# Kernel tuning notes

Hardware: AMD Instinct MI355X
Metric: run time of the kernel (lower is better)

Reference implementation:

```python
import jax, jax.numpy as jnp
import numpy as np
from jax import lax

HEAD_NUM = 16
QKV_DIM = 16
TOP_K = 2
SQRT_EMBED = 16.0   # sqrt_embedding_dim for E=256
LOGIT_CLIP = 10.0


def setup_inputs() -> dict:
    key = jax.random.key(0)
    ks = jax.random.split(key, 12)
    B, P, N1, E, HD, NE = 256, 100, 101, 256, 256, 8
    s = 0.05
    return {
        "encoded_last_node": jax.random.normal(ks[0], (B, P, E), jnp.float32),
        "attr": jax.random.uniform(ks[1], (B, P, 4), jnp.float32),
        "encoded_nodes": jax.random.normal(ks[2], (B, N1, E), jnp.float32),
        "ninf_mask": jnp.zeros((B, P, N1), jnp.float32),
        "attention_bias": jax.random.normal(ks[3], (B, P, N1), jnp.float32),
        "attention_bias1": jax.random.normal(ks[4], (B, P, N1), jnp.float32),
        "Wq_last": jax.random.normal(ks[5], (E + 4, HD), jnp.float32) * s,
        "Wk": jax.random.normal(ks[6], (E, HD), jnp.float32) * s,
        "Wv": jax.random.normal(ks[7], (E, HD), jnp.float32) * s,
        "Wg": jax.random.normal(ks[8], (HD, NE), jnp.float32) * s,
        "expert_W": jax.random.normal(ks[9], (NE, HD, E), jnp.float32) * s,
        "expert_b": jnp.zeros((NE, E), jnp.float32),
    }


def _heads(x, H, D):
    B, n, _ = x.shape
    return x.reshape(B, n, H, D).transpose(0, 2, 1, 3)  # (B,H,n,D)


def reference(encoded_last_node, attr, encoded_nodes, ninf_mask,
              attention_bias, attention_bias1, Wq_last, Wk, Wv,
              Wg, expert_W, expert_b):
    B, P, E = encoded_last_node.shape
    H, D = HEAD_NUM, QKV_DIM
    # q from [last_node ; attr], k/v from encoded_nodes (set_kv)
    q = _heads(jnp.concatenate([encoded_last_node, attr], axis=-1) @ Wq_last, H, D)
    k = _heads(encoded_nodes @ Wk, H, D)   # (B,H,N+1,D)
    v = _heads(encoded_nodes @ Wv, H, D)
    inv_sqrt_d = 1.0 / jnp.sqrt(jnp.asarray(D, jnp.float32))
    score = jnp.einsum('bhpd,bhnd->bhpn', q, k) * inv_sqrt_d
    score = score + ninf_mask[:, None, :, :]           # rank3 ninf mask
    w = jax.nn.softmax(score, axis=-1)
    out = jnp.einsum('bhpn,bhnd->bhpd', w, v)
    out_concat = out.transpose(0, 2, 1, 3).reshape(B, P, H * D)
    # --- top-k gated MoE combine (node-level routing, eval path) ---
    x = out_concat.reshape(B * P, H * D)               # tokens
    logits = x @ Wg                                    # (T, NE)
    top_v, top_i = lax.top_k(logits, TOP_K)
    top_g = jax.nn.softmax(top_v, axis=-1)
    gates = jnp.zeros_like(logits).at[
        jnp.arange(x.shape[0])[:, None], top_i].set(top_g)   # (T, NE)
    expert_out = jnp.einsum('tf,efo->teo', x, expert_W) + expert_b[None]
    mh = jnp.einsum('teo,te->to', expert_out, gates).reshape(B, P, E)
    # --- single-head pointer scores with bias + tanh clipping ---
    score2 = jnp.einsum('bpe,bne->bpn', mh, encoded_nodes)
    score2 = score2 + attention_bias + attention_bias1
    score2 = LOGIT_CLIP * jnp.tanh(score2 / SQRT_EMBED)
    probs = jax.nn.softmax(score2 + ninf_mask, axis=-1)  # (B,P,N+1)
    return probs
```

## Files before the change

### kernel.cpp

```cpp
#include <hip/hip_runtime.h>
#include <hip/hip_bf16.h>

#define B   256
#define P   100
#define N1  101
#define E   256
#define HD  256
#define H   16
#define D   16
#define NE  8
#define NTOK (B*P)
#define NKV  (B*N1)

typedef __attribute__((ext_vector_type(8))) short short8;
typedef __attribute__((ext_vector_type(4))) float f32x4;
typedef unsigned short ushort_t;

__device__ __forceinline__ unsigned short f2bf(float f) {
  unsigned int u = __float_as_uint(f);
  unsigned int r = (u + 0x7fffu + ((u >> 16) & 1u)) >> 16;
  return (unsigned short)r;
}
__device__ __forceinline__ float bf2f(unsigned short b) {
  return __uint_as_float(((unsigned int)b) << 16);
}
__device__ __forceinline__ unsigned int cvtpk(float a, float b) {
  unsigned int r;
  asm("v_cvt_pk_bf16_f32 %0, %1, %2" : "=v"(r) : "v"(a), "v"(b));
  return r;
}
__device__ __forceinline__ float lo2f(unsigned int u) {
  return __uint_as_float(u << 16);
}
__device__ __forceinline__ float hi2f(unsigned int u) {
  return __uint_as_float(u & 0xffff0000u);
}

__device__ __forceinline__ void split3_pack(const float* v, uint4& uh,
                                            uint4& um, uint4& ul) {
  unsigned int hw[4], mw[4], lw[4];
#pragma unroll
  for (int jj = 0; jj < 4; ++jj) {
    float va = v[2 * jj], vb = v[2 * jj + 1];
    unsigned int h = cvtpk(va, vb);
    float ra = va - lo2f(h), rb = vb - hi2f(h);
    unsigned int m = cvtpk(ra, rb);
    float sa = ra - lo2f(m), sb = rb - hi2f(m);
    unsigned int l = cvtpk(sa, sb);
    hw[jj] = h; mw[jj] = m; lw[jj] = l;
  }
  uh.x = hw[0]; uh.y = hw[1]; uh.z = hw[2]; uh.w = hw[3];
  um.x = mw[0]; um.y = mw[1]; um.z = mw[2]; um.w = mw[3];
  ul.x = lw[0]; ul.y = lw[1]; ul.z = lw[2]; ul.w = lw[3];
}

__global__ __launch_bounds__(256) void wsplit3_kernel(
    const float* __restrict__ W, uint4* __restrict__ Wp, int Kreal) {
  const int gid = blockIdx.x * 256 + threadIdx.x;
  const int lane = gid & 63;
  const int rest = gid >> 6;
  const int gct = rest & 15;
  const int kt = rest >> 4;
  const int k0 = kt * 32 + (lane >> 4) * 8;
  const int c = gct * 16 + (lane & 15);
  float v[8];
#pragma unroll
  for (int j = 0; j < 8; ++j) {
    int kk = k0 + j;
    v[j] = (kk < Kreal) ? W[(size_t)kk * 256 + c] : 0.f;
  }
  uint4 uh, um, ul;
  split3_pack(v, uh, um, ul);
  Wp[(size_t)(rest * 3 + 0) * 64 + lane] = uh;
  Wp[(size_t)(rest * 3 + 1) * 64 + lane] = um;
  Wp[(size_t)(rest * 3 + 2) * 64 + lane] = ul;
}

__global__ __launch_bounds__(256) void kvproj3_kernel(
    const float* __restrict__ enc, const uint4* __restrict__ Wk3,
    const uint4* __restrict__ Wv3, float* __restrict__ kout,
    float* __restrict__ vout) {
  const int KT = 8;
  const int NKG = KT * 4;
  const int RSTRIDE = KT * 12 + 1;
  __shared__ uint4 als[32 * 97];
  const int tid = threadIdx.x;
  const int row0 = blockIdx.x * 32;
  for (int i = tid; i < 32 * NKG; i += 256) {
    const int row = i >> 5;
    const int kg = i & 31;
    float v[8];
    const float4* s = (const float4*)(enc + (size_t)(row0 + row) * 256 + kg * 8);
    float4 x0 = s[0], x1 = s[1];
    v[0] = x0.x; v[1] = x0.y; v[2] = x0.z; v[3] = x0.w;
    v[4] = x1.x; v[5] = x1.y; v[6] = x1.z; v[7] = x1.w;
    uint4 uh, um, ul;
    split3_pack(v, uh, um, ul);
    const int slot = row * RSTRIDE + kg;
    als[slot] = uh;
    als[slot + NKG] = um;
    als[slot + 2 * NKG] = ul;
  }
  __syncthreads();
  const int w = tid >> 6;
  const int lane = tid & 63;
  const int lr = lane & 15;
  const int lg4 = lane >> 4;
  f32x4 acck[2][4], accv[2][4];
#pragma unroll
  for (int rt = 0; rt < 2; ++rt)
#pragma unroll
    for (int ct = 0; ct < 4; ++ct) {
      acck[rt][ct] = (f32x4){0.f, 0.f, 0.f, 0.f};
      accv[rt][ct] = (f32x4){0.f, 0.f, 0.f, 0.f};
    }
  for (int kt = 0; kt < KT; ++kt) {
    short8 ah[2], am[2], al[2];
#pragma unroll
    for (int rt = 0; rt < 2; ++rt) {
      const int base = (rt * 16 + lr) * RSTRIDE + kt * 4 + lg4;
      ah[rt] = __builtin_bit_cast(short8, als[base]);
      am[rt] = __builtin_bit_cast(short8, als[base + NKG]);
      al[rt] = __builtin_bit_cast(short8, als[base + 2 * NKG]);
    }
#pragma unroll
    for (int ct = 0; ct < 4; ++ct) {
      const int gct = w * 4 + ct;
      const size_t base = (size_t)((kt * 16 + gct) * 3) * 64 + lane;
      {
        short8 bh = __builtin_bit_cast(short8, Wk3[base]);
        short8 bm = __builtin_bit_cast(short8, Wk3[base + 64]);
        short8 bl = __builtin_bit_cast(short8, Wk3[base + 128]);
#pragma unroll
        for (int rt = 0; rt < 2; ++rt) {
          f32x4 a = acck[rt][ct];
          a = __builtin_amdgcn_mfma_f32_16x16x32_bf16(ah[rt], bh, a, 0, 0, 0);
          a = __builtin_amdgcn_mfma_f32_16x16x32_bf16(ah[rt], bm, a, 0, 0, 0);
          a = __builtin_amdgcn_mfma_f32_16x16x32_bf16(am[rt], bh, a, 0, 0, 0);
          a = __builtin_amdgcn_mfma_f32_16x16x32_bf16(am[rt], bm, a, 0, 0, 0);
          a = __builtin_amdgcn_mfma_f32_16x16x32_bf16(ah[rt], bl, a, 0, 0, 0);
          a = __builtin_amdgcn_mfma_f32_16x16x32_bf16(al[rt], bh, a, 0, 0, 0);
          acck[rt][ct] = a;
        }
      }
      {
        short8 bh = __builtin_bit_cast(short8, Wv3[base]);
        short8 bm = __builtin_bit_cast(short8, Wv3[base + 64]);
        short8 bl = __builtin_bit_cast(short8, Wv3[base + 128]);
#pragma unroll
        for (int rt = 0; rt < 2; ++rt) {
          f32x4 a = accv[rt][ct];
          a = __builtin_amdgcn_mfma_f32_16x16x32_bf16(ah[rt], bh, a, 0, 0, 0);
          a = __builtin_amdgcn_mfma_f32_16x16x32_bf16(ah[rt], bm, a, 0, 0, 0);
          a = __builtin_amdgcn_mfma_f32_16x16x32_bf16(am[rt], bh, a, 0, 0, 0);
          a = __builtin_amdgcn_mfma_f32_16x16x32_bf16(am[rt], bm, a, 0, 0, 0);
          a = __builtin_amdgcn_mfma_f32_16x16x32_bf16(ah[rt], bl, a, 0, 0, 0);
          a = __builtin_amdgcn_mfma_f32_16x16x32_bf16(al[rt], bh, a, 0, 0, 0);
          accv[rt][ct] = a;
        }
      }
    }
  }
#pragma unroll
  for (int rt = 0; rt < 2; ++rt) {
#pragma unroll
    for (int ct = 0; ct < 4; ++ct) {
      const int gct = w * 4 + ct;
#pragma unroll
      for (int reg = 0; reg < 4; ++reg) {
        const int row = row0 + rt * 16 + lg4 * 4 + reg;
        int bb = row / N1, nn = row - bb * N1;
        size_t o = (((size_t)bb * H + gct) * N1 + nn) * D + lr;
        kout[o] = acck[rt][ct][reg];
        vout[o] = accv[rt][ct][reg];
      }
    }
  }
}

template <int KT, int MODE>
__global__ __launch_bounds__(256) void proj3_kernel(
    const float* __restrict__ src, const float* __restrict__ attr,
    const uint4* __restrict__ Wp3, float* __restrict__ outp) {
  const int RSTRIDE = KT * 12 + 1;
  __shared__ uint4 als[32 * (KT * 12 + 1)];
  const int tid = threadIdx.x;
  const int row0 = blockIdx.x * 32;
  const int NKG = KT * 4;
  for (int i = tid; i < 32 * NKG; i += 256) {
    const int row = i / NKG;
    const int kg = i - row * NKG;
    float v[8];
    const int kbase = kg * 8;
    if (MODE == 0 || kbase < 256) {
      const float4* s = (const float4*)(src + (size_t)(row0 + row) * 256 + kbase);
      float4 x0 = s[0], x1 = s[1];
      v[0] = x0.x; v[1] = x0.y; v[2] = x0.z; v[3] = x0.w;
      v[4] = x1.x; v[5] = x1.y; v[6] = x1.z; v[7] = x1.w;
    } else {
#pragma unroll
      for (int j = 0; j < 8; ++j) {
        int k = kbase + j;
        v[j] = (k >= 256 && k < 260) ? attr[(size_t)(row0 + row) * 4 + (k - 256)]
                                     : 0.f;
      }
    }
    uint4 uh, um, ul;
    split3_pack(v, uh, um, ul);
    const int slot = row * RSTRIDE + kg;
    als[slot] = uh;
    als[slot + NKG] = um;
    als[slot + 2 * NKG] = ul;
  }
  __syncthreads();
  const int w = tid >> 6;
  const int lane = tid & 63;
  const int lr = lane & 15;
  const int lg4 = lane >> 4;
  f32x4 acc[2][4];
#pragma unroll
  for (int rt = 0; rt < 2; ++rt)
#pragma unroll
    for (int ct = 0; ct < 4; ++ct) acc[rt][ct] = (f32x4){0.f, 0.f, 0.f, 0.f};
  for (int kt = 0; kt < KT; ++kt) {
    short8 ah[2], am[2], al[2];
#pragma unroll
    for (int rt = 0; rt < 2; ++rt) {
      const int base = (rt * 16 + lr) * RSTRIDE + kt * 4 + lg4;
      ah[rt] = __builtin_bit_cast(short8, als[base]);
      am[rt] = __builtin_bit_cast(short8, als[base + NKG]);
      al[rt] = __builtin_bit_cast(short8, als[base + 2 * NKG]);
    }
#pragma unroll
    for (int ct = 0; ct < 4; ++ct) {
      const int gct = w * 4 + ct;
      const size_t base = (size_t)((kt * 16 + gct) * 3) * 64 + lane;
      short8 bh = __builtin_bit_cast(short8, Wp3[base]);
      short8 bm = __builtin_bit_cast(short8, Wp3[base + 64]);
      short8 bl = __builtin_bit_cast(short8, Wp3[base + 128]);
#pragma unroll
      for (int rt = 0; rt < 2; ++rt) {
        f32x4 a = acc[rt][ct];
        a = __builtin_amdgcn_mfma_f32_16x16x32_bf16(ah[rt], bh, a, 0, 0, 0);
        a = __builtin_amdgcn_mfma_f32_16x16x32_bf16(ah[rt], bm, a, 0, 0, 0);
        a = __builtin_amdgcn_mfma_f32_16x16x32_bf16(am[rt], bh, a, 0, 0, 0);
        a = __builtin_amdgcn_mfma_f32_16x16x32_bf16(am[rt], bm, a, 0, 0, 0);
        a = __builtin_amdgcn_mfma_f32_16x16x32_bf16(ah[rt], bl, a, 0, 0, 0);
        a = __builtin_amdgcn_mfma_f32_16x16x32_bf16(al[rt], bh, a, 0, 0, 0);
        acc[rt][ct] = a;
      }
    }
  }
#pragma unroll
  for (int rt = 0; rt < 2; ++rt) {
#pragma unroll
    for (int ct = 0; ct < 4; ++ct) {
      const int gct = w * 4 + ct;
#pragma unroll
      for (int reg = 0; reg < 4; ++reg) {
        const int row = row0 + rt * 16 + lg4 * 4 + reg;
        size_t o;
        if (MODE == 0) {
          int bb = row / N1, nn = row - bb * N1;
          o = (((size_t)bb * H + gct) * N1 + nn) * D + lr;
        } else {
          int bb = row / P, pp = row - bb * P;
          o = (((size_t)bb * H + gct) * P + pp) * D + lr;
        }
        outp[o] = acc[rt][ct][reg];
      }
    }
  }
}

__device__ __forceinline__ float dot16f(
    const float4& a0, const float4& a1, const float4& a2, const float4& a3,
    const float4& b0, const float4& b1, const float4& b2, const float4& b3) {
  float s = a0.x * b0.x;
  s = fmaf(a0.y, b0.y, s); s = fmaf(a0.z, b0.z, s); s = fmaf(a0.w, b0.w, s);
  s = fmaf(a1.x, b1.x, s); s = fmaf(a1.y, b1.y, s); s = fmaf(a1.z, b1.z, s);
  s = fmaf(a1.w, b1.w, s);
  s = fmaf(a2.x, b2.x, s); s = fmaf(a2.y, b2.y, s); s = fmaf(a2.z, b2.z, s);
  s = fmaf(a2.w, b2.w, s);
  s = fmaf(a3.x, b3.x, s); s = fmaf(a3.y, b3.y, s); s = fmaf(a3.z, b3.z, s);
  s = fmaf(a3.w, b3.w, s);
  return s;
}

__global__ __launch_bounds__(256) void attn_kernel(
    const float* __restrict__ q, const float* __restrict__ k,
    const float* __restrict__ v, const float* __restrict__ ninf,
    float* __restrict__ x) {
  const int b = blockIdx.x >> 3;
  const int h0 = (blockIdx.x & 7) * 2;
  __shared__ float4 kl4[2 * 208];
  __shared__ float4 vl4[2 * 208];
  const int tid = threadIdx.x;
  const int w = tid >> 6;
  const int lane = tid & 63;
  const int hh = w >> 1;
  const int h = h0 + hh;
  const int prow = (w & 1) * 64 + lane;
  const bool act = (prow < P);
  const int p = act ? prow : (P - 1);
  const float LOG2E = 1.4426950408889634f;
  const float c1 = 0.25f * LOG2E;
  const float* qb = q + (((size_t)b * H + h) * P + p) * D;
  float4 qa0 = *(const float4*)&qb[0];
  float4 qa1 = *(const float4*)&qb[4];
  float4 qa2 = *(const float4*)&qb[8];
  float4 qa3 = *(const float4*)&qb[12];
  qa0.x *= c1; qa0.y *= c1; qa0.z *= c1; qa0.w *= c1;
  qa1.x *= c1; qa1.y *= c1; qa1.z *= c1; qa1.w *= c1;
  qa2.x *= c1; qa2.y *= c1; qa2.z *= c1; qa2.w *= c1;
  qa3.x *= c1; qa3.y *= c1; qa3.z *= c1; qa3.w *= c1;
  const float* mrow = ninf + ((size_t)b * P + p) * N1;
  const float* kw = (const float*)(kl4 + hh * 208);
  const float* vw = (const float*)(vl4 + hh * 208);

  float m2 = -1e30f, l = 0.f;
  float o[16];
#pragma unroll
  for (int d = 0; d < 16; ++d) o[d] = 0.f;

#pragma unroll
  for (int ch = 0; ch < 2; ++ch) {
    const int c0 = ch ? 52 : 0;
    const int len = ch ? 49 : 52;
    const int nf4 = len * 4;
    __syncthreads();
    for (int i = tid; i < 2 * nf4; i += 256) {
      int hs = i / nf4, rem = i - hs * nf4;
      const float4* ks =
          (const float4*)(k + (((size_t)b * H + h0 + hs) * N1 + c0) * D);
      const float4* vs =
          (const float4*)(v + (((size_t)b * H + h0 + hs) * N1 + c0) * D);
      kl4[hs * 208 + rem] = ks[rem];
      vl4[hs * 208 + rem] = vs[rem];
    }
    __syncthreads();
    const int nit = len >> 2;
    float4 mk = *(const float4*)&mrow[c0];
    for (int it = 0; it < nit; ++it) {
      const int j = it * 4;
      const int nn = (it < nit - 1) ? (c0 + j + 4) : c0;
      float4 nx = *(const float4*)&mrow[nn];
      const float4* kr0 = (const float4*)&kw[(j + 0) * D];
      const float4* kr1 = (const float4*)&kw[(j + 1) * D];
      const float4* kr2 = (const float4*)&kw[(j + 2) * D];
      const float4* kr3 = (const float4*)&kw[(j + 3) * D];
      float4 k00 = kr0[0], k01 = kr0[1], k02 = kr0[2], k03 = kr0[3];
      float4 k10 = kr1[0], k11 = kr1[1], k12 = kr1[2], k13 = kr1[3];
      float4 k20 = kr2[0], k21 = kr2[1], k22 = kr2[2], k23 = kr2[3];
      float4 k30 = kr3[0], k31 = kr3[1], k32 = kr3[2], k33 = kr3[3];
      float s0 = fmaf(mk.x, LOG2E, dot16f(qa0, qa1, qa2, qa3, k00, k01, k02, k03));
      float s1 = fmaf(mk.y, LOG2E, dot16f(qa0, qa1, qa2, qa3, k10, k11, k12, k13));
      float s2 = fmaf(mk.z, LOG2E, dot16f(qa0, qa1, qa2, qa3, k20, k21, k22, k23));
      float s3 = fmaf(mk.w, LOG2E, dot16f(qa0, qa1, qa2, qa3, k30, k31, k32, k33));
      float mn = fmaxf(fmaxf(fmaxf(s0, s1), fmaxf(s2, s3)), m2);
      float sc = exp2f(m2 - mn);
      float p0 = exp2f(s0 - mn), p1 = exp2f(s1 - mn);
      float p2 = exp2f(s2 - mn), p3 = exp2f(s3 - mn);
      l = fmaf(l, sc, (p0 + p1) + (p2 + p3));
      const float4* vr0 = (const float4*)&vw[(j + 0) * D];
      const float4* vr1 = (const float4*)&vw[(j + 1) * D];
      const float4* vr2 = (const float4*)&vw[(j + 2) * D];
      const float4* vr3 = (const float4*)&vw[(j + 3) * D];
#pragma unroll
      for (int dq = 0; dq < 4; ++dq) {
        float4 v0 = vr0[dq], v1 = vr1[dq], v2 = vr2[dq], v3 = vr3[dq];
        o[4 * dq + 0] = fmaf(o[4 * dq + 0], sc,
            fmaf(p0, v0.x, fmaf(p1, v1.x, fmaf(p2, v2.x, p3 * v3.x))));
        o[4 * dq + 1] = fmaf(o[4 * dq + 1], sc,
            fmaf(p0, v0.y, fmaf(p1, v1.y, fmaf(p2, v2.y, p3 * v3.y))));
        o[4 * dq + 2] = fmaf(o[4 * dq + 2], sc,
            fmaf(p0, v0.z, fmaf(p1, v1.z, fmaf(p2, v2.z, p3 * v3.z))));
        o[4 * dq + 3] = fmaf(o[4 * dq + 3], sc,
            fmaf(p0, v0.w, fmaf(p1, v1.w, fmaf(p2, v2.w, p3 * v3.w))));
      }
      m2 = mn;
      mk = nx;
    }
  }
  {
    const float tm = mrow[100];
    const float4* kr = (const float4*)&kw[48 * D];
    float4 k0 = kr[0], k1 = kr[1], k2 = kr[2], k3 = kr[3];
    float s = fmaf(tm, LOG2E, dot16f(qa0, qa1, qa2, qa3, k0, k1, k2, k3));
    float mn = fmaxf(m2, s);
    float sc = exp2f(m2 - mn);
    float pp = exp2f(s - mn);
    l = fmaf(l, sc, pp);
    const float4* vr = (const float4*)&vw[48 * D];
#pragma unroll
    for (int dq = 0; dq < 4; ++dq) {
      float4 v0 = vr[dq];
      o[4 * dq + 0] = fmaf(o[4 * dq + 0], sc, pp * v0.x);
      o[4 * dq + 1] = fmaf(o[4 * dq + 1], sc, pp * v0.y);
      o[4 * dq + 2] = fmaf(o[4 * dq + 2], sc, pp * v0.z);
      o[4 * dq + 3] = fmaf(o[4 * dq + 3], sc, pp * v0.w);
    }
  }
  if (act) {
    const float inv = 1.f / l;
    float* xr = &x[((size_t)b * P + p) * HD + h * D];
#pragma unroll
    for (int dq = 0; dq < 4; ++dq) {
      float4 t;
      t.x = o[4 * dq + 0] * inv; t.y = o[4 * dq + 1] * inv;
      t.z = o[4 * dq + 2] * inv; t.w = o[4 * dq + 3] * inv;
      *(float4*)&xr[4 * dq] = t;
    }
  }
}

__global__ __launch_bounds__(256) void logits_top2_kernel(
    const float* __restrict__ x, const float* __restrict__ Wg,
    int* __restrict__ topi, float* __restrict__ topg,
    ushort_t* __restrict__ xsplit) {
  __shared__ float xl[32][260];
  __shared__ float wg[E * NE];
  __shared__ float lg[32][9];
  const int tid = threadIdx.x;
  const int t0 = blockIdx.x * 32;
  for (int r = 0; r < 32; ++r) {
    float val = x[(size_t)(t0 + r) * HD + tid];
    xl[r][tid] = val;
    unsigned short hi = f2bf(val);
    unsigned short lo = f2bf(val - bf2f(hi));
    xsplit[(size_t)(t0 + r) * 512 + tid] = hi;
    xsplit[(size_t)(t0 + r) * 512 + 256 + tid] = lo;
  }
  for (int i = tid; i < E * NE; i += 256) wg[i] = Wg[i];
  __syncthreads();
  const int r = tid >> 3, e = tid & 7;
  float acc = 0.f;
  for (int f = 0; f < E; ++f) acc += xl[r][f] * wg[f * NE + e];
  lg[r][e] = acc;
  __syncthreads();
  if (tid < 32) {
    float v[8];
#pragma unroll
    for (int j = 0; j < 8; ++j) v[j] = lg[tid][j];
    int i1 = 0; float v1 = v[0];
#pragma unroll
    for (int j = 1; j < 8; ++j) if (v[j] > v1) { v1 = v[j]; i1 = j; }
    int i2 = -1; float v2 = -1e30f;
#pragma unroll
    for (int j = 0; j < 8; ++j)
      if (j != i1 && v[j] > v2) { v2 = v[j]; i2 = j; }
    float ex = __expf(v2 - v1);
    float g1 = 1.f / (1.f + ex);
    float g2 = ex / (1.f + ex);
    int t = t0 + tid;
    topi[t * 2 + 0] = i1; topi[t * 2 + 1] = i2;
    topg[t * 2 + 0] = g1; topg[t * 2 + 1] = g2;
  }
}

__global__ __launch_bounds__(1024) void build_lists_kernel(
    const int* __restrict__ topi, const float* __restrict__ topg,
    int* __restrict__ list_tok, float* __restrict__ list_gate,
    int* __restrict__ counts) {
  const int e = blockIdx.x;
  const int tid = threadIdx.x;
  const int lane = tid & 63, w = tid >> 6;
  __shared__ int wsum[16];
  int running = 0;
  for (int c = 0; c < NTOK; c += 1024) {
    int t = c + tid;
    int ia = topi[t * 2 + 0], ib = topi[t * 2 + 1];
    int slot = (ia == e) ? 0 : ((ib == e) ? 1 : -1);
    int f = (slot >= 0) ? 1 : 0;
    unsigned long long m = __ballot(f);
    if (lane == 0) wsum[w] = __popcll(m);
    __syncthreads();
    int wbase = 0, total = 0;
#pragma unroll
    for (int i = 0; i < 16; ++i) {
      int s = wsum[i];
      if (i < w) wbase += s;
      total += s;
    }
    if (f) {
      int prefix = __popcll(m & ((1ull << lane) - 1ull));
      int pos = running + wbase + prefix;
      list_tok[e * NTOK + pos] = (t << 1) | slot;
      list_gate[e * NTOK + pos] = topg[t * 2 + slot];
    }
    running += total;
    __syncthreads();
  }
  if (tid == 0) counts[e] = running;
}

__global__ __launch_bounds__(256) void wsplit_kernel(
    const float* __restrict__ eW, uint4* __restrict__ Wp) {
  const int gid = blockIdx.x * 256 + threadIdx.x;
  const int lane = gid & 63;
  const int rest = gid >> 6;
  const int gct = rest & 15;
  const int kt = (rest >> 4) & 7;
  const int e = rest >> 7;
  const int kbase = kt * 32 + (lane >> 4) * 8;
  const int c = gct * 16 + (lane & 15);
  unsigned int hi[4], lo[4];
#pragma unroll
  for (int jj = 0; jj < 4; ++jj) {
    float v0 = eW[((size_t)e * HD + (kbase + 2 * jj)) * E + c];
    float v1 = eW[((size_t)e * HD + (kbase + 2 * jj + 1)) * E + c];
    unsigned int h = cvtpk(v0, v1);
    float r0 = v0 - lo2f(h), r1 = v1 - hi2f(h);
    unsigned int l = cvtpk(r0, r1);
    hi[jj] = h; lo[jj] = l;
  }
  uint4 uh, ul;
  uh.x = hi[0]; uh.y = hi[1]; uh.z = hi[2]; uh.w = hi[3];
  ul.x = lo[0]; ul.y = lo[1]; ul.z = lo[2]; ul.w = lo[3];
  Wp[(size_t)(rest * 2 + 0) * 64 + lane] = uh;
  Wp[(size_t)(rest * 2 + 1) * 64 + lane] = ul;
}

__global__ __launch_bounds__(256) void expert_gemm_kernel(
    const ushort_t* __restrict__ xsplit, const uint4* __restrict__ Wp,
    const float* __restrict__ eb, const int* __restrict__ list_tok,
    const float* __restrict__ list_gate, const int* __restrict__ counts,
    float* __restrict__ p0, float* __restrict__ p1) {
  int e = 0, t0 = -1;
  {
    int rem = blockIdx.x;
    for (int i = 0; i < NE; ++i) {
      int nt = (counts[i] + 47) / 48;
      if (rem < nt) { e = i; t0 = rem * 48; break; }
      rem -= nt;
    }
  }
  if (t0 < 0) return;
  const int cnt = counts[e];
  const int nr = min(48, cnt - t0);
  __shared__ uint4 xls[48 * 65];
  __shared__ int stok[48];
  __shared__ float sg[48];
  const int tid = threadIdx.x;
  if (tid < 48) {
    int src = e * NTOK + t0 + ((tid < nr) ? tid : 0);
    stok[tid] = list_tok[src];
    sg[tid] = (tid < nr) ? list_gate[e * NTOK + t0 + tid] : 0.f;
  }
  __syncthreads();
  for (int i = tid; i < 48 * 64; i += 256) {
    int r = i >> 6, ch = i & 63;
    const uint4* src = (const uint4*)(xsplit + (size_t)(stok[r] >> 1) * 512);
    xls[r * 65 + ch] = src[ch];
  }
  __syncthreads();
  const int w = tid >> 6;
  const int lane = tid & 63;
  const int lr = lane & 15;
  const int lg4 = lane >> 4;
  f32x4 acc[3][4];
#pragma unroll
  for (int rt = 0; rt < 3; ++rt)
#pragma unroll
    for (int ct = 0; ct < 4; ++ct) acc[rt][ct] = (f32x4){0.f, 0.f, 0.f, 0.f};

  for (int kt = 0; kt < 8; ++kt) {
    short8 afrag[3][2];
#pragma unroll
    for (int rt = 0; rt < 3; ++rt)
#pragma unroll
      for (int pl = 0; pl < 2; ++pl) {
        uint4 u = xls[(rt * 16 + lr) * 65 + pl * 32 + kt * 4 + lg4];
        afrag[rt][pl] = __builtin_bit_cast(short8, u);
      }
#pragma unroll
    for (int ct = 0; ct < 4; ++ct) {
      const int gct = w * 4 + ct;
      const size_t base = (size_t)(((e * 8 + kt) * 16 + gct) * 2) * 64 + lane;
      short8 bh = __builtin_bit_cast(short8, Wp[base]);
      short8 bl = __builtin_bit_cast(short8, Wp[base + 64]);
#pragma unroll
      for (int rt = 0; rt < 3; ++rt) {
        acc[rt][ct] = __builtin_amdgcn_mfma_f32_16x16x32_bf16(
            afrag[rt][0], bh, acc[rt][ct], 0, 0, 0);
        acc[rt][ct] = __builtin_amdgcn_mfma_f32_16x16x32_bf16(
            afrag[rt][0], bl, acc[rt][ct], 0, 0, 0);
        acc[rt][ct] = __builtin_amdgcn_mfma_f32_16x16x32_bf16(
            afrag[rt][1], bh, acc[rt][ct], 0, 0, 0);
      }
    }
  }
#pragma unroll
  for (int rt = 0; rt < 3; ++rt) {
#pragma unroll
    for (int ct = 0; ct < 4; ++ct) {
      const int col = (w * 4 + ct) * 16 + lr;
      const float bias = eb[e * E + col];
#pragma unroll
      for (int reg = 0; reg < 4; ++reg) {
        const int ridx = rt * 16 + lg4 * 4 + reg;
        if (ridx < nr) {
          const int tokw = stok[ridx];
          const float g = sg[ridx];
          float* dst = ((tokw & 1) ? p1 : p0) + (size_t)(tokw >> 1) * E + col;
          *dst = g * (acc[rt][ct][reg] + bias);
        }
      }
    }
  }
}

__global__ __launch_bounds__(256) void score2_fused_kernel(
    const float* __restrict__ p0, const float* __restrict__ p1,
    const float* __restrict__ enc, const float* __restrict__ ab,
    const float* __restrict__ ab1, const float* __restrict__ ninf,
    float* __restrict__ out) {
  const int b = blockIdx.x >> 1;
  const int half = blockIdx.x & 1;
  const int r0 = half * 50;
  __shared__ float4 mh4[50 * 64];
  const int tid = threadIdx.x;
  for (int i = tid; i < 50 * 64; i += 256) {
    int r = i >> 6, c4 = i & 63;
    size_t idx = (size_t)(b * P + r0 + r) * 64 + c4;
    float4 a = ((const float4*)p0)[idx];
    float4 c = ((const float4*)p1)[idx];
    float4 s;
    s.x = a.x + c.x; s.y = a.y + c.y; s.z = a.z + c.z; s.w = a.w + c.w;
    mh4[i] = s;
  }
  __syncthreads();
  const int w = tid >> 6;
  const int lane = tid & 63;
  const int n0 = lane;
  const int n1v = lane + 64;
  const bool has1 = (n1v < N1);
  const int n1 = has1 ? n1v : (N1 - 1);
  const float4* er0 = (const float4*)(enc + ((size_t)b * N1 + n0) * E);
  const float4* er1 = (const float4*)(enc + ((size_t)b * N1 + n1) * E);
  float acc0[13], acc1[13];
#pragma unroll
  for (int j = 0; j < 13; ++j) { acc0[j] = 0.f; acc1[j] = 0.f; }
  for (int kk = 0; kk < 64; ++kk) {
    float4 e0 = er0[kk];
    float4 e1 = er1[kk];
#pragma unroll
    for (int j = 0; j < 13; ++j) {
      const int r = w + j * 4;
      if (r < 50) {
        float4 mv = mh4[r * 64 + kk];
        acc0[j] = fmaf(mv.w, e0.w,
                  fmaf(mv.z, e0.z, fmaf(mv.y, e0.y, fmaf(mv.x, e0.x, acc0[j]))));
        acc1[j] = fmaf(mv.w, e1.w,
                  fmaf(mv.z, e1.z, fmaf(mv.y, e1.y, fmaf(mv.x, e1.x, acc1[j]))));
      }
    }
  }
#pragma unroll
  for (int j = 0; j < 13; ++j) {
    const int r = w + j * 4;
    if (r < 50) {
      const int prow = b * P + r0 + r;
      const float* arow = ab + (size_t)prow * N1;
      const float* a1row = ab1 + (size_t)prow * N1;
      const float* nrow = ninf + (size_t)prow * N1;
      float s0 = acc0[j] + arow[n0] + a1row[n0];
      float e20 = __expf(s0 * 0.125f);
      float v0 = 10.f - 20.f / (e20 + 1.f) + nrow[n0];
      float v1 = -1e30f;
      if (has1) {
        float s1 = acc1[j] + arow[n1v] + a1row[n1v];
        float e21 = __expf(s1 * 0.125f);
        v1 = 10.f - 20.f / (e21 + 1.f) + nrow[n1v];
      }
      float mx = fmaxf(v0, v1);
#pragma unroll
      for (int off = 32; off > 0; off >>= 1)
        mx = fmaxf(mx, __shfl_xor(mx, off, 64));
      float q0 = __expf(v0 - mx);
      float q1 = has1 ? __expf(v1 - mx) : 0.f;
      float sum = q0 + q1;
#pragma unroll
      for (int off = 32; off > 0; off >>= 1)
        sum += __shfl_xor(sum, off, 64);
      float inv = 1.f / sum;
      float* orow = out + (size_t)prow * N1;
      orow[n0] = q0 * inv;
      if (has1) orow[n1v] = q1 * inv;
    }
  }
}

extern "C" void kernel_launch(void* const* d_in, const int* in_sizes, int n_in,
                              void* d_out, int out_size, void* d_ws,
                              size_t ws_size, hipStream_t stream) {
  const float* eln  = (const float*)d_in[0];
  const float* attr = (const float*)d_in[1];
  const float* enc  = (const float*)d_in[2];
  const float* ninf = (const float*)d_in[3];
  const float* ab   = (const float*)d_in[4];
  const float* ab1  = (const float*)d_in[5];
  const float* Wq   = (const float*)d_in[6];
  const float* Wk   = (const float*)d_in[7];
  const float* Wv   = (const float*)d_in[8];
  const float* Wg   = (const float*)d_in[9];
  const float* eW   = (const float*)d_in[10];
  const float* eb   = (const float*)d_in[11];
  float* out = (float*)d_out;

  char* ws = (char*)d_ws;
  size_t off = 0;
  auto carve = [&](size_t bytes) {
    char* p = ws + off;
    off += (bytes + 255) & ~size_t(255);
    return p;
  };
  float* kbuf = (float*)carve(sizeof(float) * NKV * HD);
  float* vbuf = (float*)carve(sizeof(float) * NKV * HD);
  float* qbuf = (float*)carve(sizeof(float) * NTOK * HD);
  float* xbuf = (float*)carve(sizeof(float) * NTOK * HD);
  int*   topi = (int*)carve(sizeof(int) * NTOK * 2);
  float* topg = (float*)carve(sizeof(float) * NTOK * 2);
  int*   counts = (int*)carve(sizeof(int) * 16);
  int*   list_tok = (int*)carve(sizeof(int) * NE * NTOK);
  float* list_gate = (float*)carve(sizeof(float) * NE * NTOK);
  uint4* Wp  = (uint4*)carve(sizeof(ushort_t) * NE * HD * E * 2);
  uint4* Wk3 = (uint4*)carve((size_t)8 * 16 * 3 * 64 * 16);
  uint4* Wv3 = (uint4*)carve((size_t)8 * 16 * 3 * 64 * 16);
  uint4* Wq3 = (uint4*)carve((size_t)9 * 16 * 3 * 64 * 16);
  float* pp0 = kbuf;
  float* pp1 = vbuf;
  ushort_t* xsplit = (ushort_t*)qbuf;

  wsplit_kernel<<<256, 256, 0, stream>>>(eW, Wp);
  wsplit3_kernel<<<32, 256, 0, stream>>>(Wk, Wk3, 256);
  wsplit3_kernel<<<32, 256, 0, stream>>>(Wv, Wv3, 256);
  wsplit3_kernel<<<36, 256, 0, stream>>>(Wq, Wq3, 260);
  kvproj3_kernel<<<NKV / 32, 256, 0, stream>>>(enc, Wk3, Wv3, kbuf, vbuf);
  proj3_kernel<9, 1><<<NTOK / 32, 256, 0, stream>>>(eln, attr, Wq3, qbuf);
  attn_kernel<<<B * 8, 256, 0, stream>>>(qbuf, kbuf, vbuf, ninf, xbuf);
  logits_top2_kernel<<<NTOK / 32, 256, 0, stream>>>(xbuf, Wg, topi, topg,
                                                    xsplit);
  build_lists_kernel<<<NE, 1024, 0, stream>>>(topi, topg, list_tok, list_gate,
                                              counts);
  expert_gemm_kernel<<<1075, 256, 0, stream>>>(xsplit, Wp, eb, list_tok,
                                               list_gate, counts, pp0, pp1);
  score2_fused_kernel<<<512, 256, 0, stream>>>(pp0, pp1, enc, ab, ab1, ninf,
                                               out);
}
```

Measured before the change: 319.0 us.

## Merge weight-split kernels, add lazy softmax rescale, parallelize MoE list building

Four weight-preprocessing launches become one prep kernel dispatched by block index, which saves launch overhead. The attention inner loop skips the online-softmax rescale unless some lane's new max beats the running max by more than a threshold, cutting exp and multiply work. The gating logits kernel transposes Wg in shared memory for vectorized float4 dot products. The single-pass 8-block list builder is replaced by a count/scan/scatter sequence over 200 chunks, which adds parallelism but also two extra launches, and the ordering within expert lists changes.

Result: faster. 298.2 us (-6.5%).

```diff
diff --git a/kernel.cpp b/kernel.cpp
--- a/kernel.cpp
+++ b/kernel.cpp
@@ -11,6 +11,8 @@
 #define NE  8
 #define NTOK (B*P)
 #define NKV  (B*N1)
+#define NCHK 200
+#define CHKSZ 128
 
 typedef __attribute__((ext_vector_type(8))) short short8;
 typedef __attribute__((ext_vector_type(4))) float f32x4;
@@ -54,9 +56,9 @@
   ul.x = lw[0]; ul.y = lw[1]; ul.z = lw[2]; ul.w = lw[3];
 }
 
-__global__ __launch_bounds__(256) void wsplit3_kernel(
-    const float* __restrict__ W, uint4* __restrict__ Wp, int Kreal) {
-  const int gid = blockIdx.x * 256 + threadIdx.x;
+__device__ __forceinline__ void wsplit3_body(const float* __restrict__ W,
+                                             uint4* __restrict__ Wp, int Kreal,
+                                             int gid) {
   const int lane = gid & 63;
   const int rest = gid >> 6;
   const int gct = rest & 15;
@@ -74,6 +76,46 @@
   Wp[(size_t)(rest * 3 + 0) * 64 + lane] = uh;
   Wp[(size_t)(rest * 3 + 1) * 64 + lane] = um;
   Wp[(size_t)(rest * 3 + 2) * 64 + lane] = ul;
+}
+
+__global__ __launch_bounds__(256) void prep_kernel(
+    const float* __restrict__ eW, uint4* __restrict__ Wp,
+    const float* __restrict__ Wk, uint4* __restrict__ Wk3,
+    const float* __restrict__ Wv, uint4* __restrict__ Wv3,
+    const float* __restrict__ Wq, uint4* __restrict__ Wq3) {
+  const int bx = blockIdx.x;
+  const int tid = threadIdx.x;
+  if (bx < 256) {
+    const int gid = bx * 256 + tid;
+    const int lane = gid & 63;
+    const int rest = gid >> 6;
+    const int gct = rest & 15;
+    const int kt = (rest >> 4) & 7;
+    const int e = rest >> 7;
+    const int kbase = kt * 32 + (lane >> 4) * 8;
+    const int c = gct * 16 + (lane & 15);
+    unsigned int hi[4], lo[4];
+#pragma unroll
+    for (int jj = 0; jj < 4; ++jj) {
+      float v0 = eW[((size_t)e * HD + (kbase + 2 * jj)) * E + c];
+      float v1 = eW[((size_t)e * HD + (kbase + 2 * jj + 1)) * E + c];
+      unsigned int h = cvtpk(v0, v1);
+      float r0 = v0 - lo2f(h), r1 = v1 - hi2f(h);
+      unsigned int l = cvtpk(r0, r1);
+      hi[jj] = h; lo[jj] = l;
+    }
+    uint4 uh, ul;
+    uh.x = hi[0]; uh.y = hi[1]; uh.z = hi[2]; uh.w = hi[3];
+    ul.x = lo[0]; ul.y = lo[1]; ul.z = lo[2]; ul.w = lo[3];
+    Wp[(size_t)(rest * 2 + 0) * 64 + lane] = uh;
+    Wp[(size_t)(rest * 2 + 1) * 64 + lane] = ul;
+  } else if (bx < 288) {
+    wsplit3_body(Wk, Wk3, 256, (bx - 256) * 256 + tid);
+  } else if (bx < 320) {
+    wsplit3_body(Wv, Wv3, 256, (bx - 288) * 256 + tid);
+  } else {
+    wsplit3_body(Wq, Wq3, 260, (bx - 320) * 256 + tid);
+  }
 }
 
 __global__ __launch_bounds__(256) void kvproj3_kernel(
@@ -357,28 +399,47 @@
       float s1 = fmaf(mk.y, LOG2E, dot16f(qa0, qa1, qa2, qa3, k10, k11, k12, k13));
       float s2 = fmaf(mk.z, LOG2E, dot16f(qa0, qa1, qa2, qa3, k20, k21, k22, k23));
       float s3 = fmaf(mk.w, LOG2E, dot16f(qa0, qa1, qa2, qa3, k30, k31, k32, k33));
-      float mn = fmaxf(fmaxf(fmaxf(s0, s1), fmaxf(s2, s3)), m2);
-      float sc = exp2f(m2 - mn);
-      float p0 = exp2f(s0 - mn), p1 = exp2f(s1 - mn);
-      float p2 = exp2f(s2 - mn), p3 = exp2f(s3 - mn);
-      l = fmaf(l, sc, (p0 + p1) + (p2 + p3));
+      float gm = fmaxf(fmaxf(s0, s1), fmaxf(s2, s3));
       const float4* vr0 = (const float4*)&vw[(j + 0) * D];
       const float4* vr1 = (const float4*)&vw[(j + 1) * D];
       const float4* vr2 = (const float4*)&vw[(j + 2) * D];
       const float4* vr3 = (const float4*)&vw[(j + 3) * D];
-#pragma unroll
-      for (int dq = 0; dq < 4; ++dq) {
-        float4 v0 = vr0[dq], v1 = vr1[dq], v2 = vr2[dq], v3 = vr3[dq];
-        o[4 * dq + 0] = fmaf(o[4 * dq + 0], sc,
-            fmaf(p0, v0.x, fmaf(p1, v1.x, fmaf(p2, v2.x, p3 * v3.x))));
-        o[4 * dq + 1] = fmaf(o[4 * dq + 1], sc,
-            fmaf(p0, v0.y, fmaf(p1, v1.y, fmaf(p2, v2.y, p3 * v3.y))));
-        o[4 * dq + 2] = fmaf(o[4 * dq + 2], sc,
-            fmaf(p0, v0.z, fmaf(p1, v1.z, fmaf(p2, v2.z, p3 * v3.z))));
-        o[4 * dq + 3] = fmaf(o[4 * dq + 3], sc,
-            fmaf(p0, v0.w, fmaf(p1, v1.w, fmaf(p2, v2.w, p3 * v3.w))));
-      }
-      m2 = mn;
+      if (__any(gm > m2 + 8.f)) {
+        float mn = fmaxf(gm, m2);
+        float sc = exp2f(m2 - mn);
+        float p0 = exp2f(s0 - mn), p1 = exp2f(s1 - mn);
+        float p2 = exp2f(s2 - mn), p3 = exp2f(s3 - mn);
+        l = fmaf(l, sc, (p0 + p1) + (p2 + p3));
+#pragma unroll
+        for (int dq = 0; dq < 4; ++dq) {
+          float4 v0 = vr0[dq], v1 = vr1[dq], v2 = vr2[dq], v3 = vr3[dq];
+          o[4 * dq + 0] = fmaf(o[4 * dq + 0], sc,
+              fmaf(p0, v0.x, fmaf(p1, v1.x, fmaf(p2, v2.x, p3 * v3.x))));
+          o[4 * dq + 1] = fmaf(o[4 * dq + 1], sc,
+              fmaf(p0, v0.y, fmaf(p1, v1.y, fmaf(p2, v2.y, p3 * v3.y))));
+          o[4 * dq + 2] = fmaf(o[4 * dq + 2], sc,
+              fmaf(p0, v0.z, fmaf(p1, v1.z, fmaf(p2, v2.z, p3 * v3.z))));
+          o[4 * dq + 3] = fmaf(o[4 * dq + 3], sc,
+              fmaf(p0, v0.w, fmaf(p1, v1.w, fmaf(p2, v2.w, p3 * v3.w))));
+        }
+        m2 = mn;
+      } else {
+        float p0 = exp2f(s0 - m2), p1 = exp2f(s1 - m2);
+        float p2 = exp2f(s2 - m2), p3 = exp2f(s3 - m2);
+        l += (p0 + p1) + (p2 + p3);
+#pragma unroll
+        for (int dq = 0; dq < 4; ++dq) {
+          float4 v0 = vr0[dq], v1 = vr1[dq], v2 = vr2[dq], v3 = vr3[dq];
+          o[4 * dq + 0] = fmaf(p0, v0.x,
+              fmaf(p1, v1.x, fmaf(p2, v2.x, fmaf(p3, v3.x, o[4 * dq + 0]))));
+          o[4 * dq + 1] = fmaf(p0, v0.y,
+              fmaf(p1, v1.y, fmaf(p2, v2.y, fmaf(p3, v3.y, o[4 * dq + 1]))));
+          o[4 * dq + 2] = fmaf(p0, v0.z,
+              fmaf(p1, v1.z, fmaf(p2, v2.z, fmaf(p3, v3.z, o[4 * dq + 2]))));
+          o[4 * dq + 3] = fmaf(p0, v0.w,
+              fmaf(p1, v1.w, fmaf(p2, v2.w, fmaf(p3, v3.w, o[4 * dq + 3]))));
+        }
+      }
       mk = nx;
     }
   }
@@ -419,7 +480,7 @@
     int* __restrict__ topi, float* __restrict__ topg,
     ushort_t* __restrict__ xsplit) {
   __shared__ float xl[32][260];
-  __shared__ float wg[E * NE];
+  __shared__ float wgt[8 * 260];
   __shared__ float lg[32][9];
   const int tid = threadIdx.x;
   const int t0 = blockIdx.x * 32;
@@ -431,11 +492,22 @@
     xsplit[(size_t)(t0 + r) * 512 + tid] = hi;
     xsplit[(size_t)(t0 + r) * 512 + 256 + tid] = lo;
   }
-  for (int i = tid; i < E * NE; i += 256) wg[i] = Wg[i];
+  for (int i = tid; i < E * NE; i += 256) {
+    wgt[(i & 7) * 260 + (i >> 3)] = Wg[i];
+  }
   __syncthreads();
   const int r = tid >> 3, e = tid & 7;
   float acc = 0.f;
-  for (int f = 0; f < E; ++f) acc += xl[r][f] * wg[f * NE + e];
+  const float* xr = &xl[r][0];
+  const float* wr = &wgt[e * 260];
+  for (int f = 0; f < E; f += 4) {
+    float4 xv = *(const float4*)&xr[f];
+    float4 wv = *(const float4*)&wr[f];
+    acc += xv.x * wv.x;
+    acc += xv.y * wv.y;
+    acc += xv.z * wv.z;
+    acc += xv.w * wv.w;
+  }
   lg[r][e] = acc;
   __syncthreads();
   if (tid < 32) {
@@ -458,67 +530,62 @@
   }
 }
 
-__global__ __launch_bounds__(1024) void build_lists_kernel(
+__global__ __launch_bounds__(CHKSZ) void moe_count_kernel(
+    const int* __restrict__ topi, int* __restrict__ chunk_cnt) {
+  __shared__ int cnt[NE];
+  const int tid = threadIdx.x;
+  if (tid < NE) cnt[tid] = 0;
+  __syncthreads();
+  const int t = blockIdx.x * CHKSZ + tid;
+  atomicAdd(&cnt[topi[t * 2 + 0]], 1);
+  atomicAdd(&cnt[topi[t * 2 + 1]], 1);
+  __syncthreads();
+  if (tid < NE) chunk_cnt[blockIdx.x * NE + tid] = cnt[tid];
+}
+
+__global__ __launch_bounds__(64) void moe_scan_kernel(
+    const int* __restrict__ chunk_cnt, int* __restrict__ chunk_base,
+    int* __restrict__ counts) {
+  const int e = threadIdx.x;
+  if (e < NE) {
+    int run = 0;
+    for (int c = 0; c < NCHK; ++c) {
+      chunk_base[c * NE + e] = run;
+      run += chunk_cnt[c * NE + e];
+    }
+    counts[e] = run;
+  }
+}
+
+__global__ __launch_bounds__(CHKSZ) void moe_scatter_kernel(
     const int* __restrict__ topi, const float* __restrict__ topg,
-    int* __restrict__ list_tok, float* __restrict__ list_gate,
-    int* __restrict__ counts) {
-  const int e = blockIdx.x;
+    const int* __restrict__ chunk_base, int* __restrict__ list_tok,
+    float* __restrict__ list_gate) {
+  __shared__ int w0cnt[NE];
   const int tid = threadIdx.x;
-  const int lane = tid & 63, w = tid >> 6;
-  __shared__ int wsum[16];
-  int running = 0;
-  for (int c = 0; c < NTOK; c += 1024) {
-    int t = c + tid;
-    int ia = topi[t * 2 + 0], ib = topi[t * 2 + 1];
-    int slot = (ia == e) ? 0 : ((ib == e) ? 1 : -1);
-    int f = (slot >= 0) ? 1 : 0;
-    unsigned long long m = __ballot(f);
-    if (lane == 0) wsum[w] = __popcll(m);
-    __syncthreads();
-    int wbase = 0, total = 0;
-#pragma unroll
-    for (int i = 0; i < 16; ++i) {
-      int s = wsum[i];
-      if (i < w) wbase += s;
-      total += s;
-    }
-    if (f) {
-      int prefix = __popcll(m & ((1ull << lane) - 1ull));
-      int pos = running + wbase + prefix;
-      list_tok[e * NTOK + pos] = (t << 1) | slot;
-      list_gate[e * NTOK + pos] = topg[t * 2 + slot];
-    }
-    running += total;
-    __syncthreads();
-  }
-  if (tid == 0) counts[e] = running;
-}
-
-__global__ __launch_bounds__(256) void wsplit_kernel(
-    const float* __restrict__ eW, uint4* __restrict__ Wp) {
-  const int gid = blockIdx.x * 256 + threadIdx.x;
-  const int lane = gid & 63;
-  const int rest = gid >> 6;
-  const int gct = rest & 15;
-  const int kt = (rest >> 4) & 7;
-  const int e = rest >> 7;
-  const int kbase = kt * 32 + (lane >> 4) * 8;
-  const int c = gct * 16 + (lane & 15);
-  unsigned int hi[4], lo[4];
-#pragma unroll
-  for (int jj = 0; jj < 4; ++jj) {
-    float v0 = eW[((size_t)e * HD + (kbase + 2 * jj)) * E + c];
-    float v1 = eW[((size_t)e * HD + (kbase + 2 * jj + 1)) * E + c];
-    unsigned int h = cvtpk(v0, v1);
-    float r0 = v0 - lo2f(h), r1 = v1 - hi2f(h);
-    unsigned int l = cvtpk(r0, r1);
-    hi[jj] = h; lo[jj] = l;
-  }
-  uint4 uh, ul;
-  uh.x = hi[0]; uh.y = hi[1]; uh.z = hi[2]; uh.w = hi[3];
-  ul.x = lo[0]; ul.y = lo[1]; ul.z = lo[2]; ul.w = lo[3];
-  Wp[(size_t)(rest * 2 + 0) * 64 + lane] = uh;
-  Wp[(size_t)(rest * 2 + 1) * 64 + lane] = ul;
+  const int wv = tid >> 6, lane = tid & 63;
+  const int t = blockIdx.x * CHKSZ + tid;
+  const int ia = topi[t * 2 + 0], ib = topi[t * 2 + 1];
+  const float ga = topg[t * 2 + 0], gb = topg[t * 2 + 1];
+  const unsigned long long lmask = (lane == 0) ? 0ull : ((~0ull) >> (64 - lane));
+  int prefA = 0, prefB = 0;
+#pragma unroll
+  for (int e = 0; e < NE; ++e) {
+    unsigned long long mc = __ballot(ia == e) | __ballot(ib == e);
+    if (wv == 0 && lane == 0) w0cnt[e] = __popcll(mc);
+    int pref = __popcll(mc & lmask);
+    if (ia == e) prefA = pref;
+    if (ib == e) prefB = pref;
+  }
+  __syncthreads();
+  const int baseA =
+      chunk_base[blockIdx.x * NE + ia] + (wv ? w0cnt[ia] : 0) + prefA;
+  const int baseB =
+      chunk_base[blockIdx.x * NE + ib] + (wv ? w0cnt[ib] : 0) + prefB;
+  list_tok[ia * NTOK + baseA] = (t << 1) | 0;
+  list_gate[ia * NTOK + baseA] = ga;
+  list_tok[ib * NTOK + baseB] = (t << 1) | 1;
+  list_gate[ib * NTOK + baseB] = gb;
 }
 
 __global__ __launch_bounds__(256) void expert_gemm_kernel(
@@ -722,6 +789,8 @@
   int*   topi = (int*)carve(sizeof(int) * NTOK * 2);
   float* topg = (float*)carve(sizeof(float) * NTOK * 2);
   int*   counts = (int*)carve(sizeof(int) * 16);
+  int*   chunk_cnt = (int*)carve(sizeof(int) * NCHK * NE);
+  int*   chunk_base = (int*)carve(sizeof(int) * NCHK * NE);
   int*   list_tok = (int*)carve(sizeof(int) * NE * NTOK);
   float* list_gate = (float*)carve(sizeof(float) * NE * NTOK);
   uint4* Wp  = (uint4*)carve(sizeof(ushort_t) * NE * HD * E * 2);
@@ -732,17 +801,16 @@
   float* pp1 = vbuf;
   ushort_t* xsplit = (ushort_t*)qbuf;
 
-  wsplit_kernel<<<256, 256, 0, stream>>>(eW, Wp);
-  wsplit3_kernel<<<32, 256, 0, stream>>>(Wk, Wk3, 256);
-  wsplit3_kernel<<<32, 256, 0, stream>>>(Wv, Wv3, 256);
-  wsplit3_kernel<<<36, 256, 0, stream>>>(Wq, Wq3, 260);
+  prep_kernel<<<356, 256, 0, stream>>>(eW, Wp, Wk, Wk3, Wv, Wv3, Wq, Wq3);
   kvproj3_kernel<<<NKV / 32, 256, 0, stream>>>(enc, Wk3, Wv3, kbuf, vbuf);
   proj3_kernel<9, 1><<<NTOK / 32, 256, 0, stream>>>(eln, attr, Wq3, qbuf);
   attn_kernel<<<B * 8, 256, 0, stream>>>(qbuf, kbuf, vbuf, ninf, xbuf);
   logits_top2_kernel<<<NTOK / 32, 256, 0, stream>>>(xbuf, Wg, topi, topg,
                                                     xsplit);
-  build_lists_kernel<<<NE, 1024, 0, stream>>>(topi, topg, list_tok, list_gate,
-                                              counts);
+  moe_count_kernel<<<NCHK, CHKSZ, 0, stream>>>(topi, chunk_cnt);
+  moe_scan_kernel<<<1, 64, 0, stream>>>(chunk_cnt, chunk_base, counts);
+  moe_scatter_kernel<<<NCHK, CHKSZ, 0, stream>>>(topi, topg, chunk_base,
+                                                 list_tok, list_gate);
   expert_gemm_kernel<<<1075, 256, 0, stream>>>(xsplit, Wp, eb, list_tok,
                                                list_gate, counts, pp0, pp1);
   score2_fused_kernel<<<512, 256, 0, stream>>>(pp0, pp1, enc, ab, ab1, ninf,
```
